# Performance work log

Measured on AMD Instinct MI355X. Metric: run time of the kernel, lower is better.

Reference implementation:

```python
import jax, jax.numpy as jnp
import numpy as np

B, L, C_IN = 32, 1024, 64
D, H, DFF, NL = 512, 8, 2048, 3
E = D // H
K_MA = 25                      # moving-average kernel for series decomposition
TOP_K = int(1 * np.log(L))     # attention_factor * ln(L) = 6
EPS = 1e-5


def setup_inputs() -> dict:
    key = jax.random.key(0)
    ks = jax.random.split(key, 10)
    r = lambda k, sh: jax.random.normal(k, sh, jnp.float32) * 0.02
    return {
        "x": jax.random.normal(ks[0], (B, L, C_IN), jnp.float32),
        "embed_w": r(ks[1], (3, C_IN, D)),          # circular conv1d k=3, no bias
        "wq": r(ks[2], (NL, D, D)), "bq": jnp.zeros((NL, D), jnp.float32),
        "wk": r(ks[3], (NL, D, D)), "bk": jnp.zeros((NL, D), jnp.float32),
        "wv": r(ks[4], (NL, D, D)), "bv": jnp.zeros((NL, D), jnp.float32),
        "wo": r(ks[5], (NL, D, D)), "bo": jnp.zeros((NL, D), jnp.float32),
        "w1": r(ks[6], (NL, D, DFF)),               # pointwise conv1 (no bias)
        "w2": r(ks[7], (NL, DFF, D)),               # pointwise conv2 (no bias)
        "ln_g": jnp.ones((D,), jnp.float32), "ln_b": jnp.zeros((D,), jnp.float32),
        "proj_w": r(ks[8], (D, C_IN)), "proj_b": jnp.zeros((C_IN,), jnp.float32),
    }


def _series_decomp(x):
    """x - moving_average(x) with edge-replicated padding (returns residual)."""
    pad = (K_MA - 1) // 2
    xp = jnp.concatenate([jnp.repeat(x[:, :1], pad, axis=1), x,
                          jnp.repeat(x[:, -1:], pad, axis=1)], axis=1)
    cs = jnp.cumsum(xp, axis=1)
    cs = jnp.concatenate([jnp.zeros_like(cs[:, :1]), cs], axis=1)
    mean = (cs[:, K_MA:] - cs[:, :-K_MA]) / K_MA   # (B, L, D) moving average
    return x - mean


def _autocorrelation(q, k, v):
    """FFT-based AutoCorrelation attention. q,k,v: (B, L, H, E)."""
    qf = jnp.fft.rfft(q.transpose(0, 2, 3, 1), axis=-1)   # (B,H,E,Lf)
    kf = jnp.fft.rfft(k.transpose(0, 2, 3, 1), axis=-1)
    corr = jnp.fft.irfft(qf * jnp.conj(kf), n=L, axis=-1)  # (B,H,E,L)
    vals = v.transpose(0, 2, 3, 1)                          # (B,H,E,L)
    mean_corr = corr.mean(axis=(1, 2))                      # (B,L)
    w, delay = jax.lax.top_k(mean_corr, TOP_K)              # (B,K)
    tc = jax.nn.softmax(w, axis=-1)
    idx = (jnp.arange(L)[None, None, :] + delay[:, :, None]) % L      # (B,K,L)
    pat = jnp.take_along_axis(vals[:, None], idx[:, :, None, None, :], axis=-1)  # (B,K,H,E,L)
    out = jnp.einsum('bkhel,bk->bhel', pat, tc)
    return out.transpose(0, 3, 1, 2)                        # (B,L,H,E)


def reference(x, embed_w, wq, bq, wk, bk, wv, bv, wo, bo, w1, w2, ln_g, ln_b, proj_w, proj_b):
    # TokenEmbedding: circular conv1d kernel=3, no bias (dropout is identity at eval)
    xp = jnp.concatenate([x[:, -1:], x, x[:, :1]], axis=1)  # circular pad (B,L+2,C)
    h = sum(jnp.einsum('blc,cd->bld', xp[:, j:j + L], embed_w[j]) for j in range(3))
    for l in range(NL):
        q = (h @ wq[l] + bq[l]).reshape(B, L, H, E)
        k = (h @ wk[l] + bk[l]).reshape(B, L, H, E)
        v = (h @ wv[l] + bv[l]).reshape(B, L, H, E)
        a = _autocorrelation(q, k, v).reshape(B, L, D) @ wo[l] + bo[l]
        h = _series_decomp(h + a)                 # decomp1 (keep seasonal residual)
        y = jax.nn.gelu(h @ w1[l], approximate=False) @ w2[l]   # pointwise FFN
        h = _series_decomp(h + y)                 # decomp2
    # my_Layernorm: LN then subtract time-mean
    mu = h.mean(-1, keepdims=True)
    var = ((h - mu) ** 2).mean(-1, keepdims=True)
    hn = (h - mu) / jnp.sqrt(var + EPS) * ln_g + ln_b
    hn = hn - hn.mean(axis=1, keepdims=True)
    return hn @ proj_w + proj_b                   # (B, L, C_IN)
```

## Files before the change

kernel.cpp:

```cpp
#include <hip/hip_runtime.h>
#include <hip/hip_bf16.h>
#include <math.h>

#define B_   32
#define L_   1024
#define CIN_ 64
#define D_   512
#define DFF_ 2048
#define NL_  3
#define TOPK_ 6
#define NBLD_ ((size_t)B_ * L_ * D_)

#define TM 64
#define TN 64
#define TBK 16

typedef unsigned short u16;
typedef _Float16 f16x8 __attribute__((ext_vector_type(8)));
typedef float  f32x4  __attribute__((ext_vector_type(4)));

typedef const __attribute__((address_space(1))) void* gp1_t;
typedef __attribute__((address_space(3))) void* lp3_t;

__device__ __forceinline__ void gll16(const void* g, void* l) {
  __builtin_amdgcn_global_load_lds((gp1_t)g, (lp3_t)l, 16, 0, 0);
}

__device__ __forceinline__ float bf2f(u16 u) {
  return __uint_as_float(((unsigned int)u) << 16);
}
__device__ __forceinline__ u16 f2bf(float f) {
  unsigned int u = __float_as_uint(f);
  return (u16)((u + 0x7fffu + ((u >> 16) & 1u)) >> 16);
}
__device__ __forceinline__ unsigned int split2(float f) {
  u16 hi = f2bf(f);
  u16 lo = f2bf(f - bf2f(hi));
  return (unsigned int)hi | ((unsigned int)lo << 16);
}
__device__ __forceinline__ u16 f2h(float f) {
  union { _Float16 h; u16 u; } cv;
  cv.h = (_Float16)f;
  return cv.u;
}
__device__ __forceinline__ float h2f(u16 u) {
  union { u16 u; _Float16 h; } cv;
  cv.u = u;
  return (float)cv.h;
}
__device__ __forceinline__ float gelu_f(float x) {
  return 0.5f * x * (1.0f + erff(x * 0.70710678118654752440f));
}

__global__ __launch_bounds__(256) void zero_k(float* __restrict__ p, int n) {
  int i = blockIdx.x * 256 + threadIdx.x;
  if (i < n) p[i] = 0.f;
}

__global__ __launch_bounds__(256) void transp_split_k(const float* __restrict__ W,
                                                      u16* __restrict__ WTh,
                                                      u16* __restrict__ WTl,
                                                      int K, int N, int stride,
                                                      int f16_from) {
  __shared__ float tile[32][33];
  const int z = blockIdx.z;
  W   += (size_t)z * stride;
  WTh += (size_t)z * stride;
  WTl += (size_t)z * stride;
  const int t = threadIdx.x;
  const int k0 = blockIdx.x * 32, n0 = blockIdx.y * 32;
  const int tx = t & 31, ty = t >> 5;
#pragma unroll
  for (int i = 0; i < 4; ++i) {
    int kk = ty + i * 8;
    tile[kk][tx] = W[(size_t)(k0 + kk) * N + n0 + tx];
  }
  __syncthreads();
#pragma unroll
  for (int i = 0; i < 4; ++i) {
    int nn = ty + i * 8;
    float v = tile[tx][nn];
    size_t o = (size_t)(n0 + nn) * K + k0 + tx;
    if (z >= f16_from) {
      WTh[o] = f2h(v);
    } else {
      unsigned int s = split2(v);
      WTh[o] = (u16)(s & 0xffffu);
      WTl[o] = (u16)(s >> 16);
    }
  }
}

__global__ __launch_bounds__(256) void mfma_f16_gemm_k(
    const u16* __restrict__ Ah, int lda,
    const u16* __restrict__ Wh, int ldwt,
    void* __restrict__ Cv, int ldc,
    const float* __restrict__ bias,
    const u16* __restrict__ Rh, const u16* __restrict__ Rl,
    int K, int mode)
{
  __shared__ __align__(16) char smem[32768];
  u16* Ash = (u16*)smem;
  u16* Bsh = Ash + 128 * 32;
  const int t = threadIdx.x;
  const int m0 = blockIdx.x * 128, n0 = blockIdx.y * 128;
  const int lane = t & 63, w = t >> 6;
  const int lrow = lane >> 2, lq = lane & 3;
  const int qg8 = (lq ^ ((lrow >> 1) & 3)) * 8;
  const int wm = (w & 1) * 64, wn = (w >> 1) * 64;
  const int lm = lane & 15, quad = lane >> 4;
  const int kq8 = (quad ^ ((lm >> 1) & 3)) * 8;

  f32x4 acc[4][4];
#pragma unroll
  for (int i = 0; i < 4; ++i)
#pragma unroll
    for (int j = 0; j < 4; ++j) acc[i][j] = (f32x4){0.f, 0.f, 0.f, 0.f};

  for (int k0 = 0; k0 < K; k0 += 32) {
    __syncthreads();
#pragma unroll
    for (int seg = 0; seg < 2; ++seg) {
      const int r0 = w * 32 + seg * 16;
      const size_t ga = (size_t)(m0 + r0 + lrow) * lda + k0 + qg8;
      const size_t gb = (size_t)(n0 + r0 + lrow) * ldwt + k0 + qg8;
      gll16(Ah + ga, &Ash[r0 * 32]);
      gll16(Wh + gb, &Bsh[r0 * 32]);
    }
    __syncthreads();

    f16x8 af[4], bf[4];
#pragma unroll
    for (int mi = 0; mi < 4; ++mi)
      af[mi] = *(const f16x8*)&Ash[(wm + mi * 16 + lm) * 32 + kq8];
#pragma unroll
    for (int ni = 0; ni < 4; ++ni)
      bf[ni] = *(const f16x8*)&Bsh[(wn + ni * 16 + lm) * 32 + kq8];
#pragma unroll
    for (int mi = 0; mi < 4; ++mi)
#pragma unroll
      for (int ni = 0; ni < 4; ++ni)
        acc[mi][ni] = __builtin_amdgcn_mfma_f32_16x16x32_f16(af[mi], bf[ni], acc[mi][ni], 0, 0, 0);
  }

  float bcol[4];
#pragma unroll
  for (int ni = 0; ni < 4; ++ni)
    bcol[ni] = (bias && (mode == 0 || mode == 5)) ? bias[n0 + wn + ni * 16 + lm] : 0.f;
  __syncthreads();
  float* epi = (float*)smem + w * 2048;
  float* Cf = (float*)Cv;
  u16* Cu = (u16*)Cv;
#pragma unroll
  for (int mi2 = 0; mi2 < 2; ++mi2) {
#pragma unroll
    for (int mm = 0; mm < 2; ++mm) {
      int mi = mi2 * 2 + mm;
#pragma unroll
      for (int ni = 0; ni < 4; ++ni)
#pragma unroll
        for (int r = 0; r < 4; ++r)
          epi[(mm * 16 + quad * 4 + r) * 64 + ni * 16 + lm] = acc[mi][ni][r] + bcol[ni];
    }
#pragma unroll
    for (int i = 0; i < 8; ++i) {
      int f = lane + 64 * i;
      int row = f >> 4, c4 = f & 15;
      int gr = m0 + wm + mi2 * 32 + row;
      int gc = n0 + wn + c4 * 4;
      size_t ci = (size_t)gr * ldc + gc;
      float4 v = *(const float4*)&epi[row * 64 + c4 * 4];
      if (mode == 0) {
        if (Rh) {
          ushort4 rh = *(const ushort4*)&Rh[ci];
          ushort4 rl = *(const ushort4*)&Rl[ci];
          v.x += bf2f(rh.x) + bf2f(rl.x); v.y += bf2f(rh.y) + bf2f(rl.y);
          v.z += bf2f(rh.z) + bf2f(rl.z); v.w += bf2f(rh.w) + bf2f(rl.w);
        }
        *(float4*)&Cf[ci] = v;
      } else if (mode == 2) {
        float4 o = *(const float4*)&Cf[ci];
        v.x += o.x; v.y += o.y; v.z += o.z; v.w += o.w;
        *(float4*)&Cf[ci] = v;
      } else if (mode == 5) {
        ushort4 hv;
        hv.x = f2h(v.x); hv.y = f2h(v.y); hv.z = f2h(v.z); hv.w = f2h(v.w);
        *(ushort4*)&Cu[ci] = hv;
      } else {
        ushort4 hv;
        hv.x = f2h(gelu_f(v.x)); hv.y = f2h(gelu_f(v.y));
        hv.z = f2h(gelu_f(v.z)); hv.w = f2h(gelu_f(v.w));
        *(ushort4*)&Cu[ci] = hv;
      }
    }
  }
}

__global__ __launch_bounds__(256) void fftcorr_k(
    const u16* __restrict__ q, const u16* __restrict__ kv,
    float* __restrict__ Sre, float* __restrict__ Sim)
{
  __shared__ float zre[1024 * 9];
  __shared__ float zim[1024 * 9];
  __shared__ float twr[512];
  __shared__ float twi[512];
  const int t = threadIdx.x;
  const int b = blockIdx.y;
  const int d0 = blockIdx.x * 8;
  const int ch = t & 7, lidx = t >> 3;

  for (int k = t; k < 512; k += 256) {
    float ang = (float)k * 6.13592315154256e-3f;
    twr[k] = cosf(ang);
    twi[k] = -sinf(ang);
  }

  const size_t gbase = (((size_t)b << 10)) * D_ + d0 + ch;
  for (int it = 0; it < 32; ++it) {
    int l = (lidx << 5) + it;
    float qv = h2f(q[gbase + (size_t)l * D_]);
    float kw = h2f(kv[gbase + (size_t)l * D_]);
    int p = __brev((unsigned)l) >> 22;
    zre[p * 9 + ch] = qv;
    zim[p * 9 + ch] = kw;
  }
  __syncthreads();

  const int gg = t >> 3;
#pragma unroll
  for (int s = 0; s < 10; s += 2) {
    const int m = 1 << s;
#pragma unroll
    for (int it2 = 0; it2 < 8; ++it2) {
      int g = gg + (it2 << 5);
      int wi_ = g & (m - 1);
      int base = ((g >> s) << (s + 2)) | wi_;
      int i0 = (base) * 9 + ch;
      int i1 = (base + m) * 9 + ch;
      int i2 = (base + 2 * m) * 9 + ch;
      int i3 = (base + 3 * m) * 9 + ch;
      int w1x = wi_ << (9 - s);
      int w2x = wi_ << (8 - s);
      int w2y = (wi_ + m) << (8 - s);
      float w1r = twr[w1x], w1i = twi[w1x];
      float w2ar = twr[w2x], w2ai = twi[w2x];
      float w2br = twr[w2y], w2bi = twi[w2y];
      float ar = zre[i0], ai = zim[i0];
      float br = zre[i1], bi = zim[i1];
      float cr = zre[i2], ci = zim[i2];
      float dr = zre[i3], di = zim[i3];
      float t1r = br * w1r - bi * w1i, t1i = br * w1i + bi * w1r;
      float u0r = ar + t1r, u0i = ai + t1i;
      float u1r = ar - t1r, u1i = ai - t1i;
      float t3r = dr * w1r - di * w1i, t3i = dr * w1i + di * w1r;
      float u2r = cr + t3r, u2i = ci + t3i;
      float u3r = cr - t3r, u3i = ci - t3i;
      float v0r = u2r * w2ar - u2i * w2ai, v0i = u2r * w2ai + u2i * w2ar;
      float v1r = u3r * w2br - u3i * w2bi, v1i = u3r * w2bi + u3i * w2br;
      zre[i0] = u0r + v0r; zim[i0] = u0i + v0i;
      zre[i2] = u0r - v0r; zim[i2] = u0i - v0i;
      zre[i1] = u1r + v1r; zim[i1] = u1i + v1i;
      zre[i3] = u1r - v1r; zim[i3] = u1i - v1i;
    }
    __syncthreads();
  }

  for (int it = 0; it <= 16; ++it) {
    int f = gg + (it << 5);
    if (f <= 512) {
      int fm = (1024 - f) & 1023;
      float zr = zre[f * 9 + ch],  zi0 = zim[f * 9 + ch];
      float mr = zre[fm * 9 + ch], mi0 = zim[fm * 9 + ch];
      float Qr = 0.5f * (zr + mr),  Qi = 0.5f * (zi0 - mi0);
      float Kr = 0.5f * (zi0 + mi0), Ki = -0.5f * (zr - mr);
      float Pr = Qr * Kr + Qi * Ki;
      float Pi = Qi * Kr - Qr * Ki;
      Pr += __shfl_xor(Pr, 1); Pi += __shfl_xor(Pi, 1);
      Pr += __shfl_xor(Pr, 2); Pi += __shfl_xor(Pi, 2);
      Pr += __shfl_xor(Pr, 4); Pi += __shfl_xor(Pi, 4);
      if (ch == 0) {
        atomicAdd(&Sre[(b << 10) + f], Pr);
        atomicAdd(&Sim[(b << 10) + f], Pi);
      }
    }
  }
}

__global__ __launch_bounds__(256) void ifft_topk_k(
    float* __restrict__ Sre, float* __restrict__ Sim,
    float* __restrict__ tc, int* __restrict__ dly)
{
  __shared__ float re[1024], im[1024];
  __shared__ float twr[512], twi[512];
  __shared__ float rv[256];
  __shared__ int ri[256];
  __shared__ float wsel[TOPK_];
  __shared__ int dsel[TOPK_];
  const int b = blockIdx.x, t = threadIdx.x;

  for (int k = t; k < 512; k += 256) {
    float ang = (float)k * 6.13592315154256e-3f;
    twr[k] = cosf(ang);
    twi[k] = sinf(ang);
  }
  for (int l = t; l < 1024; l += 256) {
    int f = (l <= 512) ? l : 1024 - l;
    float sr = Sre[(b << 10) + f];
    float si = Sim[(b << 10) + f];
    if (l > 512) si = -si;
    int p = __brev((unsigned)l) >> 22;
    re[p] = sr; im[p] = si;
  }
  __syncthreads();
  for (int f = t; f <= 512; f += 256) {
    Sre[(b << 10) + f] = 0.f;
    Sim[(b << 10) + f] = 0.f;
  }

#pragma unroll
  for (int s = 0; s < 10; s += 2) {
    const int m = 1 << s;
    int wi_ = t & (m - 1);
    int base = ((t >> s) << (s + 2)) | wi_;
    int i0 = base, i1 = base + m, i2 = base + 2 * m, i3 = base + 3 * m;
    int w1x = wi_ << (9 - s);
    int w2x = wi_ << (8 - s);
    int w2y = (wi_ + m) << (8 - s);
    float w1r = twr[w1x], w1i = twi[w1x];
    float w2ar = twr[w2x], w2ai = twi[w2x];
    float w2br = twr[w2y], w2bi = twi[w2y];
    float ar = re[i0], ai = im[i0];
    float br = re[i1], bi = im[i1];
    float cr = re[i2], ci = im[i2];
    float dr = re[i3], di = im[i3];
    float t1r = br * w1r - bi * w1i, t1i = br * w1i + bi * w1r;
    float u0r = ar + t1r, u0i = ai + t1i;
    float u1r = ar - t1r, u1i = ai - t1i;
    float t3r = dr * w1r - di * w1i, t3i = dr * w1i + di * w1r;
    float u2r = cr + t3r, u2i = ci + t3i;
    float u3r = cr - t3r, u3i = ci - t3i;
    float v0r = u2r * w2ar - u2i * w2ai, v0i = u2r * w2ai + u2i * w2ar;
    float v1r = u3r * w2br - u3i * w2bi, v1i = u3r * w2bi + u3i * w2br;
    re[i0] = u0r + v0r; im[i0] = u0i + v0i;
    re[i2] = u0r - v0r; im[i2] = u0i - v0i;
    re[i1] = u1r + v1r; im[i1] = u1i + v1i;
    re[i3] = u1r - v1r; im[i3] = u1i - v1i;
    __syncthreads();
  }

  const float scale = 1.0f / (1024.f * 512.f);
  for (int i = t; i < 1024; i += 256) re[i] *= scale;
  __syncthreads();

  for (int kk = 0; kk < TOPK_; ++kk) {
    float bv = -INFINITY; int bi = 0x7fffffff;
    for (int i = t; i < 1024; i += 256) {
      float v = re[i];
      if (v > bv) { bv = v; bi = i; }
    }
    rv[t] = bv; ri[t] = bi;
    __syncthreads();
    for (int s2 = 128; s2 > 0; s2 >>= 1) {
      if (t < s2) {
        if (rv[t + s2] > rv[t] || (rv[t + s2] == rv[t] && ri[t + s2] < ri[t])) {
          rv[t] = rv[t + s2]; ri[t] = ri[t + s2];
        }
      }
      __syncthreads();
    }
    if (t == 0) { wsel[kk] = rv[0]; dsel[kk] = ri[0]; re[ri[0]] = -INFINITY; }
    __syncthreads();
  }
  if (t == 0) {
    float m = wsel[0];
    float e[TOPK_], se = 0.f;
    for (int k = 0; k < TOPK_; ++k) { e[k] = expf(wsel[k] - m); se += e[k]; }
    for (int k = 0; k < TOPK_; ++k) {
      tc[b * TOPK_ + k] = e[k] / se;
      dly[b * TOPK_ + k] = dsel[k];
    }
  }
}

__global__ __launch_bounds__(256) void gemm_k(
    const float* __restrict__ A, int lda,
    const float* __restrict__ W, int ldw,
    float* __restrict__ C, int ldc,
    const float* __restrict__ bias,
    int K, const float* __restrict__ mu)
{
  __shared__ float As[TBK][TM + 4];
  __shared__ float Bs[TBK][TN + 4];
  const int t = threadIdx.x;
  const int m0 = blockIdx.x * TM;
  const int n0 = blockIdx.y * TN;
  const int tx = t & 15, ty = t >> 4;
  const int ar = t >> 2, akv = (t & 3) * 4;
  const int bkk = t >> 4, bc = (t & 15) * 4;
  const int mb = (m0 + ar) >> 10;
  float acc[4][4] = {};
  for (int k0 = 0; k0 < K; k0 += TBK) {
    float4 a4 = *(const float4*)&A[(size_t)(m0 + ar) * lda + (k0 + akv)];
    float4 w4 = *(const float4*)&W[(size_t)(k0 + bkk) * ldw + (n0 + bc)];
    if (mu) {
      float4 m4 = *(const float4*)&mu[(mb << 9) + k0 + akv];
      a4.x -= m4.x; a4.y -= m4.y; a4.z -= m4.z; a4.w -= m4.w;
    }
    __syncthreads();
    As[akv + 0][ar] = a4.x; As[akv + 1][ar] = a4.y;
    As[akv + 2][ar] = a4.z; As[akv + 3][ar] = a4.w;
    *(float4*)&Bs[bkk][bc] = w4;
    __syncthreads();
#pragma unroll
    for (int kk = 0; kk < TBK; ++kk) {
      float4 a = *(const float4*)&As[kk][ty * 4];
      float4 b = *(const float4*)&Bs[kk][tx * 4];
      float av[4] = {a.x, a.y, a.z, a.w};
      float bv[4] = {b.x, b.y, b.z, b.w};
#pragma unroll
      for (int i = 0; i < 4; ++i)
#pragma unroll
        for (int j = 0; j < 4; ++j) acc[i][j] += av[i] * bv[j];
    }
  }
#pragma unroll
  for (int i = 0; i < 4; ++i) {
    int m = m0 + ty * 4 + i;
    float* crow = &C[(size_t)m * ldc + (n0 + tx * 4)];
    float4 v = make_float4(acc[i][0], acc[i][1], acc[i][2], acc[i][3]);
    if (bias) {
      const float* bp = &bias[n0 + tx * 4];
      v.x += bp[0]; v.y += bp[1]; v.z += bp[2]; v.w += bp[3];
    }
    *(float4*)crow = v;
  }
}

__global__ __launch_bounds__(256) void embed_k(
    const float* __restrict__ x, const float* __restrict__ W,
    u16* __restrict__ Ch, u16* __restrict__ Cf)
{
  __shared__ float As[TBK][TM + 4];
  __shared__ float Bs[TBK][TN + 4];
  const int t = threadIdx.x;
  const int m0 = blockIdx.x * TM, n0 = blockIdx.y * TN;
  const int tx = t & 15, ty = t >> 4;
  const int ar = t >> 2, akv = (t & 3) * 4;
  const int bkk = t >> 4, bc = (t & 15) * 4;
  const int m = m0 + ar, mb = m >> 10, ml = m & (L_ - 1);
  float acc[4][4] = {};
  for (int k0 = 0; k0 < 3 * CIN_; k0 += TBK) {
    int kcol = k0 + akv;
    int j = kcol >> 6, c = kcol & 63;
    int lsrc = (ml + j - 1 + L_) & (L_ - 1);
    float4 a4 = *(const float4*)&x[((size_t)mb * L_ + lsrc) * CIN_ + c];
    float4 w4 = *(const float4*)&W[(size_t)(k0 + bkk) * D_ + (n0 + bc)];
    __syncthreads();
    As[akv + 0][ar] = a4.x; As[akv + 1][ar] = a4.y;
    As[akv + 2][ar] = a4.z; As[akv + 3][ar] = a4.w;
    *(float4*)&Bs[bkk][bc] = w4;
    __syncthreads();
#pragma unroll
    for (int kk = 0; kk < TBK; ++kk) {
      float4 a = *(const float4*)&As[kk][ty * 4];
      float4 b = *(const float4*)&Bs[kk][tx * 4];
      float av[4] = {a.x, a.y, a.z, a.w};
      float bv[4] = {b.x, b.y, b.z, b.w};
#pragma unroll
      for (int i = 0; i < 4; ++i)
#pragma unroll
        for (int jj = 0; jj < 4; ++jj) acc[i][jj] += av[i] * bv[jj];
    }
  }
#pragma unroll
  for (int i = 0; i < 4; ++i) {
    int mm = m0 + ty * 4 + i;
    size_t ci = (size_t)mm * D_ + (n0 + tx * 4);
    ushort4 hv, lv, fv;
    unsigned int s0 = split2(acc[i][0]), s1 = split2(acc[i][1]);
    unsigned int s2 = split2(acc[i][2]), s3 = split2(acc[i][3]);
    hv.x = (u16)s0; hv.y = (u16)s1; hv.z = (u16)s2; hv.w = (u16)s3;
    lv.x = (u16)(s0 >> 16); lv.y = (u16)(s1 >> 16); lv.z = (u16)(s2 >> 16); lv.w = (u16)(s3 >> 16);
    fv.x = f2h(acc[i][0]); fv.y = f2h(acc[i][1]);
    fv.z = f2h(acc[i][2]); fv.w = f2h(acc[i][3]);
    *(ushort4*)&Ch[ci] = hv;
    *(ushort4*)&Ch[ci + NBLD_] = lv;
    *(ushort4*)&Cf[ci] = fv;
  }
}

__global__ __launch_bounds__(256) void gather_k(const float* __restrict__ v,
    const float* __restrict__ tc, const int* __restrict__ dly, u16* __restrict__ out)
{
  int tid = blockIdx.x * 256 + threadIdx.x;
  int c4 = tid & 127;
  int row = tid >> 7;
  int b = row >> 10, l = row & (L_ - 1);
  const float4* vb = (const float4*)(v + (size_t)b * L_ * D_);
  float4 o = make_float4(0.f, 0.f, 0.f, 0.f);
#pragma unroll
  for (int k = 0; k < TOPK_; ++k) {
    int ld = (l + dly[b * TOPK_ + k]) & (L_ - 1);
    float w = tc[b * TOPK_ + k];
    float4 vv = vb[(size_t)ld * (D_ / 4) + c4];
    o.x += w * vv.x; o.y += w * vv.y; o.z += w * vv.z; o.w += w * vv.w;
  }
  ushort4 hv;
  hv.x = f2h(o.x); hv.y = f2h(o.y); hv.z = f2h(o.z); hv.w = f2h(o.w);
  *(ushort4*)&out[(size_t)tid * 4] = hv;
}

__global__ __launch_bounds__(256) void decomp_k(const float* __restrict__ s,
                                                u16* __restrict__ outh,
                                                u16* __restrict__ outf)
{
  __shared__ float tile[152][64];
  const int t = threadIdx.x;
  const int l0 = blockIdx.x * 128, d0 = blockIdx.y * 64, b = blockIdx.z;
  const float* sb = s + (size_t)b * L_ * D_;
  for (int idx = t; idx < 152 * 16; idx += 256) {
    int row = idx >> 4, c4 = (idx & 15) * 4;
    int lsrc = l0 - 12 + row;
    lsrc = lsrc < 0 ? 0 : (lsrc > L_ - 1 ? L_ - 1 : lsrc);
    *(float4*)&tile[row][c4] = *(const float4*)&sb[(size_t)lsrc * D_ + d0 + c4];
  }
  __syncthreads();
  const int d = t & 63, lb = (t >> 6) * 32;
  float sum = 0.f;
#pragma unroll
  for (int j = 0; j < 25; ++j) sum += tile[lb + j][d];
  for (int it = 0; it < 32; ++it) {
    int lp = lb + it;
    float val = tile[lp + 12][d] - sum * (1.0f / 25.0f);
    unsigned int sp = split2(val);
    size_t ci = ((size_t)b * L_ + l0 + lp) * D_ + d0 + d;
    outh[ci] = (u16)(sp & 0xffffu);
    outh[ci + NBLD_] = (u16)(sp >> 16);
    outf[ci] = f2h(val);
    if (it < 31) sum += tile[lp + 25][d] - tile[lp][d];
  }
}

__global__ __launch_bounds__(256) void ln_k(const u16* __restrict__ ah,
    const float* __restrict__ g, const float* __restrict__ be, float* __restrict__ out)
{
  const int row = blockIdx.x * 4 + (threadIdx.x >> 6);
  const int lane = threadIdx.x & 63;
  const size_t base = (size_t)row * D_;
  uint4 hv = *(const uint4*)&ah[base + lane * 8];
  uint4 lv = *(const uint4*)&ah[base + lane * 8 + NBLD_];
  const unsigned int* hp = (const unsigned int*)&hv;
  const unsigned int* lp = (const unsigned int*)&lv;
  float x[8];
  float s = 0.f;
#pragma unroll
  for (int j = 0; j < 4; ++j) {
    float a0 = bf2f((u16)(hp[j] & 0xffffu)) + bf2f((u16)(lp[j] & 0xffffu));
    float a1 = bf2f((u16)(hp[j] >> 16)) + bf2f((u16)(lp[j] >> 16));
    x[2 * j] = a0; x[2 * j + 1] = a1; s += a0 + a1;
  }
#pragma unroll
  for (int o = 32; o > 0; o >>= 1) s += __shfl_xor(s, o);
  float mu = s * (1.0f / 512.0f);
  float v = 0.f;
#pragma unroll
  for (int j = 0; j < 8; ++j) { x[j] -= mu; v += x[j] * x[j]; }
#pragma unroll
  for (int o = 32; o > 0; o >>= 1) v += __shfl_xor(v, o);
  float rs = rsqrtf(v * (1.0f / 512.0f) + 1e-5f);
  float4 g0 = *(const float4*)&g[lane * 8];
  float4 g1 = *(const float4*)&g[lane * 8 + 4];
  float4 b0 = *(const float4*)&be[lane * 8];
  float4 b1 = *(const float4*)&be[lane * 8 + 4];
  float4 o0 = make_float4(x[0] * rs * g0.x + b0.x, x[1] * rs * g0.y + b0.y,
                          x[2] * rs * g0.z + b0.z, x[3] * rs * g0.w + b0.w);
  float4 o1 = make_float4(x[4] * rs * g1.x + b1.x, x[5] * rs * g1.y + b1.y,
                          x[6] * rs * g1.z + b1.z, x[7] * rs * g1.w + b1.w);
  *(float4*)&out[base + lane * 8] = o0;
  *(float4*)&out[base + lane * 8 + 4] = o1;
}

__global__ __launch_bounds__(256) void colmean_mu_k(const float* __restrict__ a,
                                                    float* __restrict__ mu)
{
  __shared__ float red[256];
  const int b = blockIdx.x, d0 = blockIdx.y * 64;
  const int d = threadIdx.x & 63, lg = threadIdx.x >> 6;
  const float* p = a + (size_t)b * L_ * D_ + d0 + d;
  float sum = 0.f;
  for (int l = lg; l < L_; l += 4) sum += p[(size_t)l * D_];
  red[threadIdx.x] = sum;
  __syncthreads();
  if (lg == 0) {
    float s = red[d] + red[d + 64] + red[d + 128] + red[d + 192];
    mu[(b << 9) + d0 + d] = s * (1.0f / 1024.0f);
  }
}

extern "C" void kernel_launch(void* const* d_in, const int* in_sizes, int n_in,
                              void* d_out, int out_size, void* d_ws, size_t ws_size,
                              hipStream_t stream) {
  (void)n_in; (void)in_sizes; (void)ws_size; (void)out_size;
  const float* x    = (const float*)d_in[0];
  const float* embw = (const float*)d_in[1];
  const float* wq   = (const float*)d_in[2];
  const float* bq   = (const float*)d_in[3];
  const float* wk   = (const float*)d_in[4];
  const float* bk   = (const float*)d_in[5];
  const float* wv   = (const float*)d_in[6];
  const float* bv   = (const float*)d_in[7];
  const float* wo   = (const float*)d_in[8];
  const float* bo   = (const float*)d_in[9];
  const float* w1   = (const float*)d_in[10];
  const float* w2   = (const float*)d_in[11];
  const float* lng  = (const float*)d_in[12];
  const float* lnb  = (const float*)d_in[13];
  const float* pw   = (const float*)d_in[14];
  const float* pb   = (const float*)d_in[15];

  const size_t nBLD = NBLD_;
  u16*   hh  = (u16*)d_ws;
  float* t0f = (float*)(hh + 2 * nBLD);
  u16*   t0h = (u16*)t0f;
  float* t1f = t0f + nBLD;
  u16*   t1h = (u16*)t1f;
  float* Sre = t1f + nBLD;
  float* Sim = Sre + (size_t)B_ * L_;
  float* tc    = Sim + (size_t)B_ * L_;
  int*   dly   = (int*)(tc + B_ * TOPK_);
  u16* base = (u16*)(dly + B_ * TOPK_ + 64);
  const size_t nDD = (size_t)NL_ * D_ * D_, nDF = (size_t)NL_ * D_ * DFF_;
  u16* wqTh = base;             u16* wqTl = wqTh + nDD;
  u16* wkTh = wqTl + nDD;       u16* wkTl = wkTh + nDD;
  u16* wvTh = wkTl + nDD;       u16* wvTl = wvTh + nDD;
  u16* woTh = wvTl + nDD;       u16* woTl = woTh + nDD;
  u16* w1Th = woTl + nDD;       u16* w1Tl = w1Th + nDF;
  u16* w2Th = w1Tl + nDF;       u16* w2Tl = w2Th + nDF;
  u16* h16 = t1h + nBLD;
  u16* qh  = t0h;
  u16* kh  = t0h + nBLD;

  dim3 blk(256);
  const dim3 gGemm(512, 8);
  const dim3 gMfma(256, 4);
  const dim3 gFft(64, B_);

  transp_split_k<<<dim3(16, 16, 3), blk, 0, stream>>>(wq, wqTh, wqTl, D_, D_, D_ * D_, 0);
  transp_split_k<<<dim3(16, 16, 3), blk, 0, stream>>>(wk, wkTh, wkTl, D_, D_, D_ * D_, 0);
  transp_split_k<<<dim3(16, 16, 3), blk, 0, stream>>>(wv, wvTh, wvTl, D_, D_, D_ * D_, 0);
  transp_split_k<<<dim3(16, 16, 3), blk, 0, stream>>>(wo, woTh, woTl, D_, D_, D_ * D_, 0);
  transp_split_k<<<dim3(16, 64, 3), blk, 0, stream>>>(w1, w1Th, w1Tl, D_, DFF_, D_ * DFF_, 0);
  transp_split_k<<<dim3(64, 16, 3), blk, 0, stream>>>(w2, w2Th, w2Tl, DFF_, D_, DFF_ * D_, 0);

  embed_k<<<gGemm, blk, 0, stream>>>(x, embw, hh, h16);
  zero_k<<<dim3(256), blk, 0, stream>>>(Sre, 2 * B_ * L_);

  for (int l = 0; l < NL_; ++l) {
    const size_t oDD = (size_t)l * D_ * D_;
    const u16* hl = hh + nBLD;

    mfma_f16_gemm_k<<<gMfma, blk, 0, stream>>>(h16, D_, wqTh + oDD, D_,
        qh, D_, bq + (size_t)l * D_, nullptr, nullptr, D_, 5);
    mfma_f16_gemm_k<<<gMfma, blk, 0, stream>>>(h16, D_, wkTh + oDD, D_,
        kh, D_, bk + (size_t)l * D_, nullptr, nullptr, D_, 5);

    fftcorr_k<<<gFft, blk, 0, stream>>>(qh, kh, Sre, Sim);
    ifft_topk_k<<<dim3(B_), blk, 0, stream>>>(Sre, Sim, tc, dly);

    mfma_f16_gemm_k<<<gMfma, blk, 0, stream>>>(h16, D_, wvTh + oDD, D_,
        t0f, D_, bv + (size_t)l * D_, nullptr, nullptr, D_, 0);
    gather_k<<<dim3(16384), blk, 0, stream>>>(t0f, tc, dly, t1h);

    mfma_f16_gemm_k<<<gMfma, blk, 0, stream>>>(t1h, D_, woTh + oDD, D_,
        t0f, D_, bo + (size_t)l * D_, hh, hl, D_, 0);
    decomp_k<<<dim3(8, 8, B_), blk, 0, stream>>>(t0f, hh, h16);

    for (int mc = 0; mc < 2; ++mc) {
      const size_t moff = (size_t)mc * 16384 * D_;
      for (int c = 0; c < 2; ++c) {
        const size_t o1 = (size_t)l * D_ * DFF_ + (size_t)c * 1024 * D_;
        const size_t o2 = (size_t)l * DFF_ * D_ + (size_t)c * 1024;
        mfma_f16_gemm_k<<<dim3(128, 8), blk, 0, stream>>>(h16 + moff, D_, w1Th + o1, D_,
            t1h, 1024, nullptr, nullptr, nullptr, D_, 4);
        if (c == 0)
          mfma_f16_gemm_k<<<dim3(128, 4), blk, 0, stream>>>(t1h, 1024, w2Th + o2, DFF_,
              t0f + moff, D_, nullptr, hh + moff, hl + moff, 1024, 0);
        else
          mfma_f16_gemm_k<<<dim3(128, 4), blk, 0, stream>>>(t1h, 1024, w2Th + o2, DFF_,
              t0f + moff, D_, nullptr, nullptr, nullptr, 1024, 2);
      }
    }
    decomp_k<<<dim3(8, 8, B_), blk, 0, stream>>>(t0f, hh, h16);
  }

  ln_k<<<dim3(B_ * L_ / 4), blk, 0, stream>>>(hh, lng, lnb, t0f);
  colmean_mu_k<<<dim3(B_, 8), blk, 0, stream>>>(t0f, t1f);
  gemm_k<<<dim3(512, 1), blk, 0, stream>>>(t0f, D_, pw, CIN_, (float*)d_out, CIN_, pb, D_, t1f);
}
```

Baseline: 2.437 ms.

## Emit Q/K projections transposed so FFT correlation reads contiguous time series

The Q and K projection GEMMs swap operands so their outputs are stored in channel-major (D, B*L) layout, with a new epilogue mode that adds the per-row bias and writes fp16. The FFT correlation kernel then loads 8 consecutive time steps per 16-byte vector instead of doing strided scalar loads across D. This is meant to cut uncoalesced global reads in the FFT stage, at the cost of a differently shaped GEMM grid whose transposed output writes may be less efficient.

```diff
diff --git a/kernel.cpp b/kernel.cpp
--- a/kernel.cpp
+++ b/kernel.cpp
@@ -10,6 +10,7 @@
 #define NL_  3
 #define TOPK_ 6
 #define NBLD_ ((size_t)B_ * L_ * D_)
+#define BL_  ((size_t)B_ * L_)
 
 #define TM 64
 #define TN 64
@@ -182,6 +183,12 @@
         float4 o = *(const float4*)&Cf[ci];
         v.x += o.x; v.y += o.y; v.z += o.z; v.w += o.w;
         *(float4*)&Cf[ci] = v;
+      } else if (mode == 6) {
+        float br = bias ? bias[gr] : 0.f;
+        ushort4 hv;
+        hv.x = f2h(v.x + br); hv.y = f2h(v.y + br);
+        hv.z = f2h(v.z + br); hv.w = f2h(v.w + br);
+        *(ushort4*)&Cu[ci] = hv;
       } else if (mode == 5) {
         ushort4 hv;
         hv.x = f2h(v.x); hv.y = f2h(v.y); hv.z = f2h(v.z); hv.w = f2h(v.w);
@@ -215,14 +222,20 @@
     twi[k] = -sinf(ang);
   }
 
-  const size_t gbase = (((size_t)b << 10)) * D_ + d0 + ch;
-  for (int it = 0; it < 32; ++it) {
-    int l = (lidx << 5) + it;
-    float qv = h2f(q[gbase + (size_t)l * D_]);
-    float kw = h2f(kv[gbase + (size_t)l * D_]);
-    int p = __brev((unsigned)l) >> 22;
-    zre[p * 9 + ch] = qv;
-    zim[p * 9 + ch] = kw;
+  const size_t gbase = (size_t)(d0 + ch) * BL_ + ((size_t)b << 10) + ((size_t)lidx << 5);
+#pragma unroll
+  for (int v = 0; v < 4; ++v) {
+    uint4 qq = *(const uint4*)&q[gbase + v * 8];
+    uint4 kk = *(const uint4*)&kv[gbase + v * 8];
+    const u16* qp = (const u16*)&qq;
+    const u16* kp = (const u16*)&kk;
+#pragma unroll
+    for (int jj = 0; jj < 8; ++jj) {
+      int l = (lidx << 5) + v * 8 + jj;
+      int p = __brev((unsigned)l) >> 22;
+      zre[p * 9 + ch] = h2f(qp[jj]);
+      zim[p * 9 + ch] = h2f(kp[jj]);
+    }
   }
   __syncthreads();
 
@@ -643,6 +656,7 @@
   dim3 blk(256);
   const dim3 gGemm(512, 8);
   const dim3 gMfma(256, 4);
+  const dim3 gMfmaT(4, 256);
   const dim3 gFft(64, B_);
 
   transp_split_k<<<dim3(16, 16, 3), blk, 0, stream>>>(wq, wqTh, wqTl, D_, D_, D_ * D_, 0);
@@ -659,10 +673,10 @@
     const size_t oDD = (size_t)l * D_ * D_;
     const u16* hl = hh + nBLD;
 
-    mfma_f16_gemm_k<<<gMfma, blk, 0, stream>>>(h16, D_, wqTh + oDD, D_,
-        qh, D_, bq + (size_t)l * D_, nullptr, nullptr, D_, 5);
-    mfma_f16_gemm_k<<<gMfma, blk, 0, stream>>>(h16, D_, wkTh + oDD, D_,
-        kh, D_, bk + (size_t)l * D_, nullptr, nullptr, D_, 5);
+    mfma_f16_gemm_k<<<gMfmaT, blk, 0, stream>>>(wqTh + oDD, D_, h16, D_,
+        qh, (int)BL_, bq + (size_t)l * D_, nullptr, nullptr, D_, 6);
+    mfma_f16_gemm_k<<<gMfmaT, blk, 0, stream>>>(wkTh + oDD, D_, h16, D_,
+        kh, (int)BL_, bk + (size_t)l * D_, nullptr, nullptr, D_, 6);
 
     fftcorr_k<<<gFft, blk, 0, stream>>>(qh, kh, Sre, Sim);
     ifft_topk_k<<<dim3(B_), blk, 0, stream>>>(Sre, Sim, tc, dly);
```

Result: slower. 2.500 ms (+2.6%).
